# Performance work log

Measured on AMD Instinct MI355X. Metric: run time of the kernel, lower is better.

## Reference

```python
import jax, jax.numpy as jnp
import numpy as np

B, T, C = 2, 2048, 1024
N_HEADS = 16
HEAD_DIM = C // N_HEADS

def setup_inputs() -> dict:
    key = jax.random.key(0)
    k1, k2, k3 = jax.random.split(key, 3)
    x = jax.random.normal(k1, (B, T, C), dtype=jnp.float32)
    W_qkv = jax.random.normal(k2, (C, 3 * C), dtype=jnp.float32) * (1.0 / np.sqrt(C))
    W_out = jax.random.normal(k3, (C, C), dtype=jnp.float32) * (1.0 / np.sqrt(C))
    return {"x": x, "W_qkv": W_qkv, "W_out": W_out}

def reference(x, W_qkv, W_out):
    b, t, c = x.shape
    qkv = jnp.einsum('btc,cd->btd', x, W_qkv)  # [B,T,3C]
    q, k, v = jnp.split(qkv, 3, axis=-1)
    # [B, H, T, hd]
    q = q.reshape(b, t, N_HEADS, HEAD_DIM).transpose(0, 2, 1, 3)
    k = k.reshape(b, t, N_HEADS, HEAD_DIM).transpose(0, 2, 1, 3)
    v = v.reshape(b, t, N_HEADS, HEAD_DIM).transpose(0, 2, 1, 3)
    scale = 1.0 / jnp.sqrt(jnp.asarray(HEAD_DIM, dtype=x.dtype))
    attn = jnp.einsum('bhqd,bhkd->bhqk', q, k) * scale  # [B,H,T,T]
    causal = jnp.tril(jnp.ones((t, t), dtype=bool))
    attn = jnp.where(causal, attn, jnp.asarray(-1e9, dtype=attn.dtype))
    attn = jax.nn.softmax(attn, axis=-1)
    out = jnp.einsum('bhqk,bhkd->bhqd', attn, v)
    out = out.transpose(0, 2, 1, 3).reshape(b, t, c)
    return jnp.einsum('btc,cd->btd', out, W_out)
```

## Files before the change

kernel.cpp:

```cpp
#include <hip/hip_runtime.h>
#include <hip/hip_bf16.h>

typedef __attribute__((ext_vector_type(8))) short short8;
typedef __attribute__((ext_vector_type(4))) short bf16x4;
typedef __attribute__((ext_vector_type(4))) float floatx4;

#define T_SEQ 2048
#define NH    16
#define HD    64
#define QSCALE 0.18033688f

#define MFMA16(a, b, c) __builtin_amdgcn_mfma_f32_16x16x16bf16_1k(a, b, c, 0, 0, 0)
#define MFMA32(a, b, c) __builtin_amdgcn_mfma_f32_16x16x32_bf16(a, b, c, 0, 0, 0)

__device__ __forceinline__ ushort f2bf(float f) {
    union { float f; unsigned u; } un; un.f = f;
    unsigned r = un.u + 0x7fff + ((un.u >> 16) & 1);
    return (ushort)(r >> 16);
}
__device__ __forceinline__ unsigned pkbf(float a, float b) {
    __hip_bfloat162 t = __float22bfloat162_rn(float2{a, b});
    return *reinterpret_cast<unsigned*>(&t);
}

typedef const __attribute__((address_space(1))) unsigned int* gp1_t;
typedef __attribute__((address_space(3))) unsigned int* lp3_t;
__device__ __forceinline__ void gl_lds16(const ushort* g, ushort* l) {
    __builtin_amdgcn_global_load_lds((gp1_t)g, (lp3_t)l, 16, 0, 0);
}

__global__ void prep_kernel(const float* __restrict__ Wqkv, const float* __restrict__ Wout,
                            const float* __restrict__ x, ushort* __restrict__ wt_qkv,
                            ushort* __restrict__ wt_out, ushort* __restrict__ x_bf) {
    __shared__ ushort tile[32][33];
    const int bid = blockIdx.x;
    if (bid >= 4096) {
        size_t i = ((size_t)(bid - 4096) * 256 + threadIdx.x) * 8;
        float4 f0 = *(const float4*)(x + i);
        float4 f1 = *(const float4*)(x + i + 4);
        short8 v;
        v[0] = (short)f2bf(f0.x); v[1] = (short)f2bf(f0.y);
        v[2] = (short)f2bf(f0.z); v[3] = (short)f2bf(f0.w);
        v[4] = (short)f2bf(f1.x); v[5] = (short)f2bf(f1.y);
        v[6] = (short)f2bf(f1.z); v[7] = (short)f2bf(f1.w);
        *(short8*)(x_bf + i) = v;
        return;
    }
    const float* in; ushort* out; int R, C, gx, gy;
    if (bid < 3072) { in = Wqkv; out = wt_qkv; R = 1024; C = 3072; gx = bid % 96; gy = bid / 96; }
    else            { int t = bid - 3072; in = Wout; out = wt_out; R = 1024; C = 1024; gx = t & 31; gy = t >> 5; }
    const int tx = threadIdx.x & 31, ty = threadIdx.x >> 5;
    const int bx = gx * 32, by = gy * 32;
    #pragma unroll
    for (int i = ty; i < 32; i += 8)
        tile[i][tx] = f2bf(in[(size_t)(by + i) * C + bx + tx]);
    __syncthreads();
    #pragma unroll
    for (int i = ty; i < 32; i += 8)
        out[(size_t)(bx + i) * R + by + tx] = tile[tx][i];
}

template <int EPI>
__global__ __launch_bounds__(256, 2)
void gemm_bt(const ushort* __restrict__ A, const ushort* __restrict__ Bt,
             void* __restrict__ O0, ushort* __restrict__ O1, ushort* __restrict__ O2,
             int M, int N, int K) {
    __shared__ __align__(16) ushort smem[8704];
    ushort* As = smem;
    ushort* Bs = smem + 4096;
    const int tid  = threadIdx.x;
    const int wave = tid >> 6, lane = tid & 63;
    const int quad = lane >> 4, l16 = lane & 15;
    const int wm = (wave >> 1) * 64, wn = (wave & 1) * 64;
    const int m0 = blockIdx.x * 128, n0 = blockIdx.y * 128;

    const int c0 = tid, c1 = tid + 256;
    const int row0 = c0 >> 2, row1 = c1 >> 2;
    const int g0 = (((c0 & 3) ^ ((row0 >> 1) & 3))) * 8;
    const int g1 = (((c1 & 3) ^ ((row1 >> 1) & 3))) * 8;
    const ushort* aP0 = A  + (size_t)(m0 + row0) * K + g0;
    const ushort* aP1 = A  + (size_t)(m0 + row1) * K + g1;
    const ushort* bP0 = Bt + (size_t)(n0 + row0) * K + g0;
    const ushort* bP1 = Bt + (size_t)(n0 + row1) * K + g1;

    floatx4 acc[4][4];
    #pragma unroll
    for (int i = 0; i < 4; i++)
        #pragma unroll
        for (int j = 0; j < 4; j++)
            acc[i][j] = (floatx4){0.f, 0.f, 0.f, 0.f};

    const int col_sw = (quad ^ ((l16 >> 1) & 3)) * 8;

    for (int k0 = 0; k0 < K; k0 += 32) {
        __syncthreads();
        gl_lds16(aP0 + k0, &As[c0 * 8]);
        gl_lds16(aP1 + k0, &As[c1 * 8]);
        gl_lds16(bP0 + k0, &Bs[c0 * 8]);
        gl_lds16(bP1 + k0, &Bs[c1 * 8]);
        __syncthreads();
        short8 af[4], bf[4];
        #pragma unroll
        for (int i = 0; i < 4; i++)
            af[i] = *(const short8*)(&As[(wm + i * 16 + l16) * 32 + col_sw]);
        #pragma unroll
        for (int j = 0; j < 4; j++)
            bf[j] = *(const short8*)(&Bs[(wn + j * 16 + l16) * 32 + col_sw]);
        #pragma unroll
        for (int i = 0; i < 4; i++)
            #pragma unroll
            for (int j = 0; j < 4; j++)
                acc[i][j] = __builtin_amdgcn_mfma_f32_16x16x32_bf16(af[i], bf[j], acc[i][j], 0, 0, 0);
    }

    if (EPI == 0 && n0 >= 2048) {
        const int b = m0 >> 11;
        const int t0 = m0 & 2047;
        const int head0 = (n0 - 2048) >> 6;
        __syncthreads();
        #pragma unroll
        for (int nh = 0; nh < 2; nh++) {
            if ((wave & 1) == nh) {
                #pragma unroll
                for (int j = 0; j < 4; j++)
                    #pragma unroll
                    for (int i = 0; i < 4; i++) {
                        int nl = j * 16 + l16;
                        int mB = wm + i * 16 + quad * 4;
                        *(unsigned*)(&smem[nl * 136 + mB])     = pkbf(acc[i][j][0], acc[i][j][1]);
                        *(unsigned*)(&smem[nl * 136 + mB + 2]) = pkbf(acc[i][j][2], acc[i][j][3]);
                    }
            }
            __syncthreads();
            #pragma unroll
            for (int cc = 0; cc < 4; cc++) {
                int c = cc * 256 + tid;
                int row = c >> 4, mcol = (c & 15) * 8;
                uint4 v = *(const uint4*)(&smem[row * 136 + mcol]);
                *(uint4*)(&O2[((size_t)(b * NH + head0 + nh) * HD + row) * T_SEQ + t0 + mcol]) = v;
            }
            __syncthreads();
        }
        return;
    }

    #pragma unroll
    for (int i = 0; i < 4; i++) {
        #pragma unroll
        for (int j = 0; j < 4; j++) {
            #pragma unroll
            for (int r = 0; r < 4; r++) {
                int m = m0 + wm + i * 16 + quad * 4 + r;
                int n = n0 + wn + j * 16 + l16;
                if (EPI == 0) {
                    int b = m >> 11, t = m & 2047;
                    int part = n >> 10, c = n & 1023;
                    int head = c >> 6, off = c & 63;
                    float av = acc[i][j][r];
                    if (part == 0) av *= QSCALE;
                    ushort v = f2bf(av);
                    if (part == 0) ((ushort*)O0)[(((size_t)(b * NH + head)) * T_SEQ + t) * HD + off] = v;
                    else           O1[(((size_t)(b * NH + head)) * T_SEQ + t) * HD + off] = v;
                } else {
                    ((float*)O0)[(size_t)m * N + n] = acc[i][j][r];
                }
            }
        }
    }
}

__device__ __forceinline__ void softmax_step(floatx4 s[4], float& mst, float& ll,
                                             floatx4 o[4], bf16x4 pf[4]) {
    float t0 = fmaxf(fmaxf(s[0][0], s[0][1]), fmaxf(s[0][2], s[0][3]));
    float t1 = fmaxf(fmaxf(s[1][0], s[1][1]), fmaxf(s[1][2], s[1][3]));
    float t2 = fmaxf(fmaxf(s[2][0], s[2][1]), fmaxf(s[2][2], s[2][3]));
    float t3 = fmaxf(fmaxf(s[3][0], s[3][1]), fmaxf(s[3][2], s[3][3]));
    float t  = fmaxf(fmaxf(t0, t1), fmaxf(t2, t3));
    if (!__all(t - mst <= 8.0f)) {
        t = fmaxf(t, __shfl_xor(t, 16));
        t = fmaxf(t, __shfl_xor(t, 32));
        float mnew  = fmaxf(mst, t);
        float alpha = exp2f(mst - mnew);
        mst = mnew;
        ll  *= alpha;
        #pragma unroll
        for (int db = 0; db < 4; db++)
            #pragma unroll
            for (int r = 0; r < 4; r++) o[db][r] *= alpha;
    }
    #pragma unroll
    for (int j = 0; j < 4; j++) {
        float p0 = exp2f(s[j][0] - mst);
        float p1 = exp2f(s[j][1] - mst);
        float p2 = exp2f(s[j][2] - mst);
        float p3 = exp2f(s[j][3] - mst);
        ll += (p0 + p1) + (p2 + p3);
        union { bf16x4 v; unsigned u[2]; } pu;
        pu.u[0] = pkbf(p0, p1);
        pu.u[1] = pkbf(p2, p3);
        pf[j] = pu.v;
    }
}

__global__ __launch_bounds__(256, 2)
void attn_kernel(const ushort* __restrict__ Q, const ushort* __restrict__ Kk,
                 const ushort* __restrict__ Vt, ushort* __restrict__ Oout) {
    __shared__ __align__(16) ushort Ks[2][128 * 64];
    __shared__ __align__(16) ushort Vs[2][64 * 128];
    const int tid  = threadIdx.x;
    const int wave = tid >> 6, lane = tid & 63;
    const int quad = lane >> 4, l16 = lane & 15;
    const int idx = blockIdx.x;
    const int bh = idx & 31;
    const int jp = idx >> 5;
    const int p  = (jp < 8) ? jp : (15 - (jp - 8));
    const int qtA = p, qtB = 31 - p;
    const int b = bh >> 4, h = bh & 15;

    const ushort* qp = Q  + (size_t)bh * T_SEQ * HD;
    const ushort* kp = Kk + (size_t)bh * T_SEQ * HD;
    const ushort* vp = Vt + (size_t)bh * HD * T_SEQ;

    const int q0A = qtA * 64 + wave * 16;
    const int q0B = qtB * 64 + wave * 16;

    short8 qfA[2], qfB[2];
    #pragma unroll
    for (int kb = 0; kb < 2; kb++) {
        qfA[kb] = *(const short8*)(qp + (size_t)(q0A + l16) * HD + kb * 32 + quad * 8);
        qfB[kb] = *(const short8*)(qp + (size_t)(q0B + l16) * HD + kb * 32 + quad * 8);
    }

    floatx4 oA[4], oB[4];
    #pragma unroll
    for (int db = 0; db < 4; db++) {
        oA[db] = (floatx4){0.f, 0.f, 0.f, 0.f};
        oB[db] = (floatx4){0.f, 0.f, 0.f, 0.f};
    }
    float mA = -1e30f, llA = 0.f, mB = -1e30f, llB = 0.f;

    int koff[4], voff[4];
    #pragma unroll
    for (int j = 0; j < 4; j++) {
        int c = tid + j * 256;
        int kr = c >> 3;
        koff[j] = kr * HD + (((c & 7) ^ (kr & 7)) * 8);
        int vr = c >> 4;
        voff[j] = vr * T_SEQ + ((((c & 15) ^ (vr & 7))) * 8);
    }

#define STAGE(BUF, I)                                                            \
    {                                                                            \
        const ushort* kg = kp + (size_t)(I) * 128 * HD;                          \
        const ushort* vg = vp + (I) * 128;                                       \
        gl_lds16(kg + koff[0], &Ks[BUF][(tid      ) * 8]);                       \
        gl_lds16(kg + koff[1], &Ks[BUF][(tid + 256) * 8]);                       \
        gl_lds16(kg + koff[2], &Ks[BUF][(tid + 512) * 8]);                       \
        gl_lds16(kg + koff[3], &Ks[BUF][(tid + 768) * 8]);                       \
        gl_lds16(vg + voff[0], &Vs[BUF][(tid      ) * 8]);                       \
        gl_lds16(vg + voff[1], &Vs[BUF][(tid + 256) * 8]);                       \
        gl_lds16(vg + voff[2], &Vs[BUF][(tid + 512) * 8]);                       \
        gl_lds16(vg + voff[3], &Vs[BUF][(tid + 768) * 8]);                       \
    }

    const int xsw = (l16 & 7), qh = quad >> 1, ql = quad & 1;
    const int ka0 = l16 * 64 + ((quad ^ xsw) * 8);
    const int ka1 = l16 * 64 + (((4 + quad) ^ xsw) * 8);
    int va[4];
    #pragma unroll
    for (int jj = 0; jj < 4; jj++)
        va[jj] = l16 * 128 + (((2 * jj + qh) ^ xsw) * 8) + ql * 4;

#define SUBCOMP(BUF, ST, KT)                                                     \
    {                                                                            \
        const int kt_ = (KT);                                                    \
        if (kt_ <= qtA) {                                                        \
            floatx4 sA[4], sB[4];                                                \
            _Pragma("unroll")                                                    \
            for (int jj = 0; jj < 4; jj++) {                                     \
                sA[jj] = (floatx4){0.f, 0.f, 0.f, 0.f};                          \
                sB[jj] = (floatx4){0.f, 0.f, 0.f, 0.f};                          \
            }                                                                    \
            __builtin_amdgcn_s_setprio(1);                                       \
            _Pragma("unroll")                                                    \
            for (int jj = 0; jj < 4; jj++) {                                     \
                short8 kf0 = *(const short8*)(&Ks[BUF][(ST) * 4096 + jj * 1024 + ka0]); \
                sB[jj] = MFMA32(kf0, qfB[0], sB[jj]);                            \
                sA[jj] = MFMA32(kf0, qfA[0], sA[jj]);                            \
            }                                                                    \
            _Pragma("unroll")                                                    \
            for (int jj = 0; jj < 4; jj++) {                                     \
                short8 kf1 = *(const short8*)(&Ks[BUF][(ST) * 4096 + jj * 1024 + ka1]); \
                sB[jj] = MFMA32(kf1, qfB[1], sB[jj]);                            \
                sA[jj] = MFMA32(kf1, qfA[1], sA[jj]);                            \
            }                                                                    \
            __builtin_amdgcn_s_setprio(0);                                       \
            if (kt_ == qtA) {                                                    \
                _Pragma("unroll")                                                \
                for (int jj = 0; jj < 4; jj++)                                   \
                    _Pragma("unroll")                                            \
                    for (int rr = 0; rr < 4; rr++)                               \
                        if (jj * 16 + quad * 4 + rr > wave * 16 + l16)           \
                            sA[jj][rr] = -1e30f;                                 \
            }                                                                    \
            bf16x4 pfA[4], pfB[4];                                               \
            softmax_step(sB, mB, llB, oB, pfB);                                  \
            softmax_step(sA, mA, llA, oA, pfA);                                  \
            __builtin_amdgcn_s_setprio(1);                                       \
            _Pragma("unroll")                                                    \
            for (int jj = 0; jj < 4; jj++)                                       \
                _Pragma("unroll")                                                \
                for (int db = 0; db < 4; db++) {                                 \
                    bf16x4 vf = *(const bf16x4*)(&Vs[BUF][va[jj] + (ST) * 64 + db * 2048]); \
                    oB[db] = MFMA16(vf, pfB[jj], oB[db]);                        \
                    oA[db] = MFMA16(vf, pfA[jj], oA[db]);                        \
                }                                                                \
            __builtin_amdgcn_s_setprio(0);                                       \
        } else {                                                                 \
            floatx4 sB[4];                                                       \
            _Pragma("unroll")                                                    \
            for (int jj = 0; jj < 4; jj++) sB[jj] = (floatx4){0.f, 0.f, 0.f, 0.f}; \
            __builtin_amdgcn_s_setprio(1);                                       \
            _Pragma("unroll")                                                    \
            for (int jj = 0; jj < 4; jj++) {                                     \
                short8 kf0 = *(const short8*)(&Ks[BUF][(ST) * 4096 + jj * 1024 + ka0]); \
                sB[jj] = MFMA32(kf0, qfB[0], sB[jj]);                            \
            }                                                                    \
            _Pragma("unroll")                                                    \
            for (int jj = 0; jj < 4; jj++) {                                     \
                short8 kf1 = *(const short8*)(&Ks[BUF][(ST) * 4096 + jj * 1024 + ka1]); \
                sB[jj] = MFMA32(kf1, qfB[1], sB[jj]);                            \
            }                                                                    \
            __builtin_amdgcn_s_setprio(0);                                       \
            if (kt_ == qtB) {                                                    \
                _Pragma("unroll")                                                \
                for (int jj = 0; jj < 4; jj++)                                   \
                    _Pragma("unroll")                                            \
                    for (int rr = 0; rr < 4; rr++)                               \
                        if (jj * 16 + quad * 4 + rr > wave * 16 + l16)           \
                            sB[jj][rr] = -1e30f;                                 \
            }                                                                    \
            bf16x4 pfB[4];                                                       \
            softmax_step(sB, mB, llB, oB, pfB);                                  \
            __builtin_amdgcn_s_setprio(1);                                       \
            _Pragma("unroll")                                                    \
            for (int jj = 0; jj < 4; jj++)                                       \
                _Pragma("unroll")                                                \
                for (int db = 0; db < 4; db++) {                                 \
                    bf16x4 vf = *(const bf16x4*)(&Vs[BUF][va[jj] + (ST) * 64 + db * 2048]); \
                    oB[db] = MFMA16(vf, pfB[jj], oB[db]);                        \
                }                                                                \
            __builtin_amdgcn_s_setprio(0);                                       \
        }                                                                        \
    }

#define ITER(BUF, I)                                                             \
    {                                                                            \
        __syncthreads();                                                         \
        if ((I) + 1 < NT) STAGE((BUF) ^ 1, (I) + 1)                              \
        SUBCOMP(BUF, 0, 2 * (I))                                                 \
        {                                                                        \
            const int kt1 = 2 * (I) + 1;                                         \
            if (kt1 <= qtB) SUBCOMP(BUF, 1, kt1)                                 \
        }                                                                        \
    }

    const int NT = (qtB + 2) >> 1;
    STAGE(0, 0)

    int i = 0;
    for (; i + 1 < NT; i += 2) {
        ITER(0, i)
        ITER(1, i + 1)
    }
    if (i < NT) ITER(0, i)
#undef ITER
#undef SUBCOMP
#undef STAGE

    {
        float lB = llB;
        lB += __shfl_xor(lB, 16);
        lB += __shfl_xor(lB, 32);
        const float inv = 1.0f / lB;
        const int t = q0B + l16;
        #pragma unroll
        for (int db = 0; db < 4; db++) {
            union { ushort4 w; unsigned u[2]; } ou;
            ou.u[0] = pkbf(oB[db][0] * inv, oB[db][1] * inv);
            ou.u[1] = pkbf(oB[db][2] * inv, oB[db][3] * inv);
            *(ushort4*)(Oout + (((size_t)b * T_SEQ + t) * NH + h) * HD + db * 16 + quad * 4) = ou.w;
        }
    }
    {
        float lA = llA;
        lA += __shfl_xor(lA, 16);
        lA += __shfl_xor(lA, 32);
        const float inv = 1.0f / lA;
        const int t = q0A + l16;
        #pragma unroll
        for (int db = 0; db < 4; db++) {
            union { ushort4 w; unsigned u[2]; } ou;
            ou.u[0] = pkbf(oA[db][0] * inv, oA[db][1] * inv);
            ou.u[1] = pkbf(oA[db][2] * inv, oA[db][3] * inv);
            *(ushort4*)(Oout + (((size_t)b * T_SEQ + t) * NH + h) * HD + db * 16 + quad * 4) = ou.w;
        }
    }
}

extern "C" void kernel_launch(void* const* d_in, const int* in_sizes, int n_in,
                              void* d_out, int out_size, void* d_ws, size_t ws_size,
                              hipStream_t stream) {
    const float* x    = (const float*)d_in[0];
    const float* Wqkv = (const float*)d_in[1];
    const float* Wout = (const float*)d_in[2];
    ushort* ws = (ushort*)d_ws;

    ushort* wt_qkv = ws;
    ushort* wt_out = wt_qkv + 3072 * 1024;
    ushort* q_ws   = wt_out + 1024 * 1024;
    ushort* k_ws   = q_ws + 4194304;
    ushort* v_t    = k_ws + 4194304;
    ushort* a_out  = v_t + 4194304;
    ushort* x_bf   = a_out + 4194304;

    prep_kernel<<<dim3(6144), 256, 0, stream>>>(Wqkv, Wout, x, wt_qkv, wt_out, x_bf);

    gemm_bt<0><<<dim3(32, 24), 256, 0, stream>>>(x_bf, wt_qkv, q_ws, k_ws, v_t, 4096, 3072, 1024);

    attn_kernel<<<dim3(512), 256, 0, stream>>>(q_ws, k_ws, v_t, a_out);

    gemm_bt<1><<<dim3(32, 8), 256, 0, stream>>>(a_out, wt_out, (float*)d_out, nullptr, nullptr,
                                                4096, 1024, 1024);
}
```

Baseline: 180.0 us.

## Batch QK^T for both sub-tiles before softmax and PV in attention loop

Restructures the per-iteration attention body so the QK^T MFMAs for both 32-key sub-tiles (and both query tiles A/B) are issued back to back, followed by masking, then softmax and PV for each. The goal is a longer independent MFMA stream that hides LDS latency and softmax dependency stalls, and fewer priority toggles. It needs more live score registers (four score sets), which raises VGPR pressure and may reduce occupancy. The PV products also lose their interleaving of A and B tiles.

```diff
diff --git a/kernel.cpp b/kernel.cpp
--- a/kernel.cpp
+++ b/kernel.cpp
@@ -271,98 +271,84 @@
     for (int jj = 0; jj < 4; jj++)
         va[jj] = l16 * 128 + (((2 * jj + qh) ^ xsw) * 8) + ql * 4;
 
-#define SUBCOMP(BUF, ST, KT)                                                     \
-    {                                                                            \
-        const int kt_ = (KT);                                                    \
-        if (kt_ <= qtA) {                                                        \
-            floatx4 sA[4], sB[4];                                                \
+#define ZS(S) { _Pragma("unroll") for (int z = 0; z < 4; z++) S[z] = (floatx4){0.f, 0.f, 0.f, 0.f}; }
+
+#define QKD(SB, SA, BUF, ST)                                                     \
+    {                                                                            \
+        _Pragma("unroll")                                                        \
+        for (int jj = 0; jj < 4; jj++) {                                         \
+            short8 kf = *(const short8*)(&Ks[BUF][(ST) * 4096 + jj * 1024 + ka0]); \
+            SB[jj] = MFMA32(kf, qfB[0], SB[jj]);                                 \
+            SA[jj] = MFMA32(kf, qfA[0], SA[jj]);                                 \
+        }                                                                        \
+        _Pragma("unroll")                                                        \
+        for (int jj = 0; jj < 4; jj++) {                                         \
+            short8 kf = *(const short8*)(&Ks[BUF][(ST) * 4096 + jj * 1024 + ka1]); \
+            SB[jj] = MFMA32(kf, qfB[1], SB[jj]);                                 \
+            SA[jj] = MFMA32(kf, qfA[1], SA[jj]);                                 \
+        }                                                                        \
+    }
+
+#define QK1(SB, BUF, ST)                                                         \
+    {                                                                            \
+        _Pragma("unroll")                                                        \
+        for (int jj = 0; jj < 4; jj++) {                                         \
+            short8 kf = *(const short8*)(&Ks[BUF][(ST) * 4096 + jj * 1024 + ka0]); \
+            SB[jj] = MFMA32(kf, qfB[0], SB[jj]);                                 \
+        }                                                                        \
+        _Pragma("unroll")                                                        \
+        for (int jj = 0; jj < 4; jj++) {                                         \
+            short8 kf = *(const short8*)(&Ks[BUF][(ST) * 4096 + jj * 1024 + ka1]); \
+            SB[jj] = MFMA32(kf, qfB[1], SB[jj]);                                 \
+        }                                                                        \
+    }
+
+#define MASKD(S)                                                                 \
+    {                                                                            \
+        _Pragma("unroll")                                                        \
+        for (int jj = 0; jj < 4; jj++)                                           \
             _Pragma("unroll")                                                    \
-            for (int jj = 0; jj < 4; jj++) {                                     \
-                sA[jj] = (floatx4){0.f, 0.f, 0.f, 0.f};                          \
-                sB[jj] = (floatx4){0.f, 0.f, 0.f, 0.f};                          \
+            for (int rr = 0; rr < 4; rr++)                                       \
+                if (jj * 16 + quad * 4 + rr > wave * 16 + l16) S[jj][rr] = -1e30f; \
+    }
+
+#define PVG(O, PF, BUF, ST)                                                      \
+    {                                                                            \
+        _Pragma("unroll")                                                        \
+        for (int jj = 0; jj < 4; jj++)                                           \
+            _Pragma("unroll")                                                    \
+            for (int db = 0; db < 4; db++) {                                     \
+                bf16x4 vf = *(const bf16x4*)(&Vs[BUF][va[jj] + (ST) * 64 + db * 2048]); \
+                O[db] = MFMA16(vf, PF[jj], O[db]);                               \
             }                                                                    \
-            __builtin_amdgcn_s_setprio(1);                                       \
-            _Pragma("unroll")                                                    \
-            for (int jj = 0; jj < 4; jj++) {                                     \
-                short8 kf0 = *(const short8*)(&Ks[BUF][(ST) * 4096 + jj * 1024 + ka0]); \
-                sB[jj] = MFMA32(kf0, qfB[0], sB[jj]);                            \
-                sA[jj] = MFMA32(kf0, qfA[0], sA[jj]);                            \
-            }                                                                    \
-            _Pragma("unroll")                                                    \
-            for (int jj = 0; jj < 4; jj++) {                                     \
-                short8 kf1 = *(const short8*)(&Ks[BUF][(ST) * 4096 + jj * 1024 + ka1]); \
-                sB[jj] = MFMA32(kf1, qfB[1], sB[jj]);                            \
-                sA[jj] = MFMA32(kf1, qfA[1], sA[jj]);                            \
-            }                                                                    \
-            __builtin_amdgcn_s_setprio(0);                                       \
-            if (kt_ == qtA) {                                                    \
-                _Pragma("unroll")                                                \
-                for (int jj = 0; jj < 4; jj++)                                   \
-                    _Pragma("unroll")                                            \
-                    for (int rr = 0; rr < 4; rr++)                               \
-                        if (jj * 16 + quad * 4 + rr > wave * 16 + l16)           \
-                            sA[jj][rr] = -1e30f;                                 \
-            }                                                                    \
-            bf16x4 pfA[4], pfB[4];                                               \
-            softmax_step(sB, mB, llB, oB, pfB);                                  \
-            softmax_step(sA, mA, llA, oA, pfA);                                  \
-            __builtin_amdgcn_s_setprio(1);                                       \
-            _Pragma("unroll")                                                    \
-            for (int jj = 0; jj < 4; jj++)                                       \
-                _Pragma("unroll")                                                \
-                for (int db = 0; db < 4; db++) {                                 \
-                    bf16x4 vf = *(const bf16x4*)(&Vs[BUF][va[jj] + (ST) * 64 + db * 2048]); \
-                    oB[db] = MFMA16(vf, pfB[jj], oB[db]);                        \
-                    oA[db] = MFMA16(vf, pfA[jj], oA[db]);                        \
-                }                                                                \
-            __builtin_amdgcn_s_setprio(0);                                       \
-        } else {                                                                 \
-            floatx4 sB[4];                                                       \
-            _Pragma("unroll")                                                    \
-            for (int jj = 0; jj < 4; jj++) sB[jj] = (floatx4){0.f, 0.f, 0.f, 0.f}; \
-            __builtin_amdgcn_s_setprio(1);                                       \
-            _Pragma("unroll")                                                    \
-            for (int jj = 0; jj < 4; jj++) {                                     \
-                short8 kf0 = *(const short8*)(&Ks[BUF][(ST) * 4096 + jj * 1024 + ka0]); \
-                sB[jj] = MFMA32(kf0, qfB[0], sB[jj]);                            \
-            }                                                                    \
-            _Pragma("unroll")                                                    \
-            for (int jj = 0; jj < 4; jj++) {                                     \
-                short8 kf1 = *(const short8*)(&Ks[BUF][(ST) * 4096 + jj * 1024 + ka1]); \
-                sB[jj] = MFMA32(kf1, qfB[1], sB[jj]);                            \
-            }                                                                    \
-            __builtin_amdgcn_s_setprio(0);                                       \
-            if (kt_ == qtB) {                                                    \
-                _Pragma("unroll")                                                \
-                for (int jj = 0; jj < 4; jj++)                                   \
-                    _Pragma("unroll")                                            \
-                    for (int rr = 0; rr < 4; rr++)                               \
-                        if (jj * 16 + quad * 4 + rr > wave * 16 + l16)           \
-                            sB[jj][rr] = -1e30f;                                 \
-            }                                                                    \
-            bf16x4 pfB[4];                                                       \
-            softmax_step(sB, mB, llB, oB, pfB);                                  \
-            __builtin_amdgcn_s_setprio(1);                                       \
-            _Pragma("unroll")                                                    \
-            for (int jj = 0; jj < 4; jj++)                                       \
-                _Pragma("unroll")                                                \
-                for (int db = 0; db < 4; db++) {                                 \
-                    bf16x4 vf = *(const bf16x4*)(&Vs[BUF][va[jj] + (ST) * 64 + db * 2048]); \
-                    oB[db] = MFMA16(vf, pfB[jj], oB[db]);                        \
-                }                                                                \
-            __builtin_amdgcn_s_setprio(0);                                       \
-        }                                                                        \
     }
 
 #define ITER(BUF, I)                                                             \
     {                                                                            \
         __syncthreads();                                                         \
         if ((I) + 1 < NT) STAGE((BUF) ^ 1, (I) + 1)                              \
-        SUBCOMP(BUF, 0, 2 * (I))                                                 \
-        {                                                                        \
-            const int kt1 = 2 * (I) + 1;                                         \
-            if (kt1 <= qtB) SUBCOMP(BUF, 1, kt1)                                 \
+        const int kt0 = 2 * (I), kt1 = kt0 + 1;                                  \
+        const bool v1 = (kt1 <= qtB);                                            \
+        const bool a0 = (kt0 <= qtA), a1 = (kt1 <= qtA);                         \
+        floatx4 sB0[4], sB1[4], sA0[4], sA1[4];                                  \
+        bf16x4 pfB0[4], pfB1[4], pfA0[4], pfA1[4];                               \
+        __builtin_amdgcn_s_setprio(1);                                           \
+        ZS(sB0)                                                                  \
+        if (a0) { ZS(sA0) QKD(sB0, sA0, BUF, 0) } else { QK1(sB0, BUF, 0) }      \
+        if (v1) {                                                                \
+            ZS(sB1)                                                              \
+            if (a1) { ZS(sA1) QKD(sB1, sA1, BUF, 1) } else { QK1(sB1, BUF, 1) }  \
         }                                                                        \
+        __builtin_amdgcn_s_setprio(0);                                           \
+        if (kt0 == qtB) { MASKD(sB0) }                                           \
+        if (v1 && kt1 == qtB) { MASKD(sB1) }                                     \
+        if (a0 && kt0 == qtA) { MASKD(sA0) }                                     \
+        if (a1 && kt1 == qtA) { MASKD(sA1) }                                     \
+        softmax_step(sB0, mB, llB, oB, pfB0);                                    \
+        PVG(oB, pfB0, BUF, 0)                                                    \
+        if (v1) { softmax_step(sB1, mB, llB, oB, pfB1); PVG(oB, pfB1, BUF, 1) }  \
+        if (a0) { softmax_step(sA0, mA, llA, oA, pfA0); PVG(oA, pfA0, BUF, 0) }  \
+        if (a1) { softmax_step(sA1, mA, llA, oA, pfA1); PVG(oA, pfA1, BUF, 1) }  \
     }
 
     const int NT = (qtB + 2) >> 1;
@@ -375,7 +361,11 @@
     }
     if (i < NT) ITER(0, i)
 #undef ITER
-#undef SUBCOMP
+#undef PVG
+#undef MASKD
+#undef QK1
+#undef QKD
+#undef ZS
 #undef STAGE
 
     {
```

Result: no change. 179.7 us (-0.2%).
